# Kernel tuning notes

Measured on AMD Instinct MI355X. Metric: run time of the kernel, lower is better.

Reference implementation:

```python
import jax, jax.numpy as jnp
import numpy as np

L = 2        # NUM_DECODER_LAYERS
D = 512      # D_MODEL == ENCODER_EMBEDDING_DIM == DECODER_EMBEDDING_DIM == DECODER_HIDDEN_DIM
T = 32       # max_trg_len (greedy decode steps)
SOS = 1      # SPECIAL_TOKENS.index('[SOS]'), PAD assumed 0


def setup_inputs() -> dict:
    key = jax.random.key(0)
    ks = jax.random.split(key, 12)
    Vin, Vout, B, S = 32000, 32000, 32, 512
    s = 0.02
    src = jax.random.randint(ks[0], (B, S), 0, Vin)
    src_emb_table = jax.random.normal(ks[1], (Vin, D), dtype=jnp.float32) * s
    trg_emb_table = (jax.random.normal(ks[2], (Vout, D), dtype=jnp.float32) * s).at[0].set(0.0)  # padding_idx=0
    Wih = jax.random.normal(ks[3], (L, 4 * D, D), dtype=jnp.float32) * s
    Whh = jax.random.normal(ks[4], (L, 4 * D, D), dtype=jnp.float32) * s
    bih = jnp.zeros((L, 4 * D), jnp.float32)
    bhh = jnp.zeros((L, 4 * D), jnp.float32)
    Wfc = jax.random.normal(ks[5], (D, D), dtype=jnp.float32) * s      # Decoder.fc_out (hid_dim -> hid_dim)
    bfc = jnp.zeros((D,), jnp.float32)
    Wh2o = jax.random.normal(ks[6], (D, 2 * D), dtype=jnp.float32) * s  # hidden_to_out
    bh2o = jnp.zeros((D,), jnp.float32)
    bout = jnp.zeros((Vout,), jnp.float32)                              # out_layer bias (weight tied to trg_emb_table)
    return dict(src=src, src_emb_table=src_emb_table, trg_emb_table=trg_emb_table,
                Wih=Wih, Whh=Whh, bih=bih, bhh=bhh, Wfc=Wfc, bfc=bfc,
                Wh2o=Wh2o, bh2o=bh2o, bout=bout)


def reference(src, src_emb_table, trg_emb_table, Wih, Whh, bih, bhh, Wfc, bfc, Wh2o, bh2o, bout):
    B, S = src.shape
    dtype = src_emb_table.dtype
    scale = jnp.asarray(D ** 0.5, dtype)
    src_e = src_emb_table[src]  # [B,S,D] -- encoder LSTM hidden/cell are computed but discarded in the original

    def lstm_cell(x, h, c, l):
        g = x @ Wih[l].T + bih[l] + h @ Whh[l].T + bhh[l]
        i, f, gg, o = jnp.split(g, 4, axis=-1)  # torch gate order i,f,g,o
        c2 = jax.nn.sigmoid(f) * c + jax.nn.sigmoid(i) * jnp.tanh(gg)
        h2 = jax.nn.sigmoid(o) * jnp.tanh(c2)
        return h2, c2

    def outer_step(carry, t):
        # Original re-runs the decoder LSTM over the whole generated prefix every
        # step, starting from the carried hidden state; we mask positions > t.
        tokens, h, c = carry  # tokens [B,T+1] int32, h/c [L,B,D]
        emb = jnp.swapaxes(trg_emb_table[tokens[:, :T]], 0, 1)  # [T,B,D]

        def pos_step(hc, inp):
            h, c = hc
            x, pos = inp
            active = pos <= t
            hs, cs = [], []
            for l in range(L):
                h2, c2 = lstm_cell(x, h[l], c[l], l)
                h2 = jnp.where(active, h2, h[l])
                c2 = jnp.where(active, c2, c[l])
                hs.append(h2); cs.append(c2)
                x = h2
            h, c = jnp.stack(hs), jnp.stack(cs)
            return (h, c), h[-1]

        (h, c), h_top = jax.lax.scan(pos_step, (h, c), (emb, jnp.arange(T)))
        out_seq = h_top @ Wfc.T + bfc                 # [T,B,D] Decoder.fc_out
        out_t = jnp.take(out_seq, t, axis=0)          # last valid position (concat[:, -1])
        w = jax.nn.softmax(jnp.einsum('bd,bsd->bs', out_t, src_e) / scale, axis=-1)
        context = jnp.einsum('bs,bsd->bd', w, src_e)
        hid = jax.nn.relu(jnp.concatenate([out_t, context], axis=-1) @ Wh2o.T + bh2o)
        logits = hid @ trg_emb_table.T + bout         # out_layer tied to decoder embedding
        nxt = jnp.argmax(logits, axis=-1).astype(tokens.dtype)
        tokens = tokens.at[:, t + 1].set(nxt)
        return (tokens, h, c), out_seq

    tokens0 = jnp.zeros((B, T + 1), jnp.int32).at[:, 0].set(SOS)
    h0 = jnp.zeros((L, B, D), dtype)
    (tokens, _, _), out_seqs = jax.lax.scan(outer_step, (tokens0, h0, h0), jnp.arange(T))
    # attn returned by the original is from the LAST decode step, queries = all T positions
    attn = jax.nn.softmax(jnp.einsum('tbd,bsd->bts', out_seqs[-1], src_e) / scale, axis=-1)  # [B,T,S]
    return tokens[:, 1:], attn
```

## Files before the change

### kernel.cpp

```cpp
#include <hip/hip_runtime.h>
#include <math.h>

#define NWG 256
#define TPB 512
#define AGT __HIP_MEMORY_SCOPE_AGENT

static constexpr int Bb = 32, Dd = 512, Tt = 32, Vv = 32000;
static constexpr int BD = Bb * Dd;
static constexpr float SCALE_INV = 0.04419417382415922f;

static constexpr size_t OFF_H0 = 4096;
static constexpr size_t OFF_H1 = OFF_H0 + 2 * (size_t)BD;
static constexpr size_t OFF_P  = OFF_H1 + 2 * (size_t)BD;
static constexpr size_t OFF_HL = OFF_P + (size_t)Tt * Bb * 2048;
static constexpr size_t OFF_HD = OFF_HL + (size_t)Tt * BD;
static constexpr size_t OFF_OF = OFF_HD + BD;
static constexpr size_t OFF_CV = OFF_OF + (size_t)Tt * BD;
static constexpr size_t OFF_CI = OFF_CV + 32 * 256;
static constexpr size_t OFF_ET = OFF_CI + 32 * 256;

static constexpr int L_W   = 0;
static constexpr int L_H   = 13824;
static constexpr int L_SC  = 30208;
static constexpr int L_RB  = 30720;
static constexpr int L_IB  = 31744;
static constexpr int L_RED = 32256;
static constexpr int L_GV  = 32272;
static constexpr int L_GI  = 32400;
static constexpr int L_TOK = 32528;
static constexpr int LDS_FLOATS = 32560;
static constexpr size_t LDS_BYTES = (size_t)LDS_FLOATS * 4;

__device__ __forceinline__ float sigm(float x) { return 1.0f / (1.0f + expf(-x)); }

__device__ __forceinline__ float ldcv(const float* p) {
  unsigned u = __hip_atomic_load((const unsigned*)p, __ATOMIC_RELAXED, AGT);
  return __builtin_bit_cast(float, u);
}
__device__ __forceinline__ void stcv(float* p, float v) {
  __hip_atomic_store((unsigned*)p, __builtin_bit_cast(unsigned, v), __ATOMIC_RELAXED, AGT);
}
__device__ __forceinline__ float2 ldcv2(const float* p) {
  unsigned long long u = __hip_atomic_load((const unsigned long long*)p, __ATOMIC_RELAXED, AGT);
  return __builtin_bit_cast(float2, u);
}
__device__ __forceinline__ int ldcvi(const int* p) {
  return (int)__hip_atomic_load((const unsigned*)p, __ATOMIC_RELAXED, AGT);
}
__device__ __forceinline__ void stcvi(int* p, int v) {
  __hip_atomic_store((unsigned*)p, (unsigned)v, __ATOMIC_RELAXED, AGT);
}

__device__ __forceinline__ float wredsum(float v) {
#pragma unroll
  for (int off = 32; off > 0; off >>= 1) v += __shfl_xor(v, off, 64);
  return v;
}

__device__ __forceinline__ void gbar(unsigned* sb, unsigned& lg) {
  const unsigned tgt = lg + 1u;
  asm volatile("s_waitcnt vmcnt(0)" ::: "memory");
  __syncthreads();
  if (threadIdx.x == 0) {
    const int g = (int)blockIdx.x >> 5;
    unsigned a = __hip_atomic_fetch_add(&sb[g * 64], 1u, __ATOMIC_RELAXED, AGT);
    if (a == 31u) {
      __hip_atomic_store(&sb[g * 64], 0u, __ATOMIC_RELAXED, AGT);
      unsigned r = __hip_atomic_fetch_add(&sb[1024], 1u, __ATOMIC_RELAXED, AGT);
      if (r == 7u) {
        __hip_atomic_store(&sb[1024], 0u, __ATOMIC_RELAXED, AGT);
#pragma unroll
        for (int gg = 0; gg < 8; ++gg)
          __hip_atomic_store(&sb[2048 + gg * 64], tgt, __ATOMIC_RELAXED, AGT);
      }
    }
    while (__hip_atomic_load(&sb[2048 + g * 64], __ATOMIC_RELAXED, AGT) < tgt)
      __builtin_amdgcn_s_sleep(1);
  }
  lg = tgt;
  __syncthreads();
}

__device__ __forceinline__ float blockMax(float v, float* red, int tid) {
#pragma unroll
  for (int off = 32; off > 0; off >>= 1) v = fmaxf(v, __shfl_xor(v, off, 64));
  if ((tid & 63) == 0) red[tid >> 6] = v;
  __syncthreads();
  float m = red[0];
#pragma unroll
  for (int i = 1; i < 8; ++i) m = fmaxf(m, red[i]);
  __syncthreads();
  return m;
}

__device__ __forceinline__ float blockSum(float v, float* red, int tid) {
  v = wredsum(v);
  if ((tid & 63) == 0) red[tid >> 6] = v;
  __syncthreads();
  float s = 0.f;
#pragma unroll
  for (int i = 0; i < 8; ++i) s += red[i];
  __syncthreads();
  return s;
}

__device__ void stageW(int wg, int tid, const float* __restrict__ Wih,
                       const float* __restrict__ Whh, float* __restrict__ SMW) {
  for (int e = tid; e < 3 * 8 * 512; e += TPB) {
    const int k = e & 511, jl = (e >> 9) & 7, m = e >> 12;
    const int q = jl >> 1, dl = jl & 1;
    const int j = q * 512 + wg * 2 + dl;
    const float* srcp = (m == 0) ? (Whh + (size_t)j * 512)
                     : (m == 1) ? (Wih + (size_t)2048 * 512 + (size_t)j * 512)
                                : (Whh + (size_t)2048 * 512 + (size_t)j * 512);
    SMW[(m * 8 + jl) * 576 + (k >> 5) * 36 + (k & 31)] = srcp[k];
  }
  __syncthreads();
}

__device__ void buildETb(int wg, int tid, const float* __restrict__ Etrg,
                         float* __restrict__ ETb, float* __restrict__ SM) {
  if (wg < 250) {
    for (int tile = 0; tile < 8; ++tile) {
      const int tv = tile >> 2, tk = tile & 3;
      __syncthreads();
      for (int e = tid; e < 64 * 128; e += TPB) {
        const int vl = e >> 7, kl = e & 127;
        SM[vl * 129 + kl] = Etrg[(size_t)(wg * 128 + tv * 64 + vl) * 512 + tk * 128 + kl];
      }
      __syncthreads();
      for (int e = tid; e < 32 * 128; e += TPB) {
        const int vp = e >> 7, kl = e & 127;
        const int v = wg * 128 + tv * 64 + vp * 2;
        const int k = tk * 128 + kl;
        float2 val = make_float2(SM[(vp * 2) * 129 + kl], SM[(vp * 2 + 1) * 129 + kl]);
        *(float2*)(ETb + ((size_t)(v >> 1) * 512 + k) * 2) = val;
      }
    }
    __syncthreads();
  }
}

__device__ __forceinline__ void phaseAB(
    int wg, int tid, bool doA, bool doB,
    const float* __restrict__ H0r, float* __restrict__ H0w,
    const float* __restrict__ H1r, float* __restrict__ H1w,
    float* __restrict__ HlP, const float* __restrict__ Pp,
    const float* __restrict__ bs1,
    const float* __restrict__ SMW, float* __restrict__ LH, float& c0, float& c1)
{
  const int kc = tid & 15, b = tid >> 4;
  float4 s0[8], s1[8];
  __builtin_amdgcn_sched_barrier(0);
  {
    const float* p0 = H0r + tid * 4;
#pragma unroll
    for (int r = 0; r < 8; ++r) {
      const float* q = p0 + r * 2048;
      asm volatile("global_load_dwordx4 %0, %1, off sc1" : "=v"(s0[r]) : "v"(q));
    }
  }
  if (doB) {
    const float* p1 = H1r + tid * 4;
#pragma unroll
    for (int r = 0; r < 8; ++r) {
      const float* q = p1 + r * 2048;
      asm volatile("global_load_dwordx4 %0, %1, off sc1" : "=v"(s1[r]) : "v"(q));
    }
  }
  __builtin_amdgcn_sched_barrier(0);
  asm volatile("s_waitcnt vmcnt(0)" ::: "memory");
  __builtin_amdgcn_sched_barrier(0);
#pragma unroll
  for (int r = 0; r < 8; ++r) {
    int byte = (r * 512 + tid) * 16;
    byte ^= ((byte >> 7) & 7) << 4;
    *(float4*)((char*)LH + byte) = s0[r];
  }
  __syncthreads();
  float4 hq[8];
#pragma unroll
  for (int j = 0; j < 8; ++j) {
    int byte = tid * 128 + j * 16;
    byte ^= ((byte >> 7) & 7) << 4;
    hq[j] = *(const float4*)((const char*)LH + byte);
  }
  if (doB) {
    __syncthreads();
#pragma unroll
    for (int r = 0; r < 8; ++r) {
      int byte = (r * 512 + tid) * 16;
      byte ^= ((byte >> 7) & 7) << 4;
      *(float4*)((char*)LH + byte) = s1[r];
    }
  }
  float accA[8], accB[8];
#pragma unroll
  for (int r = 0; r < 8; ++r) { accA[r] = 0.f; accB[r] = 0.f; }
  if (doA) {
#pragma unroll
    for (int r = 0; r < 8; ++r) {
      const float4* wr = (const float4*)(SMW + r * 576 + kc * 36);
#pragma unroll
      for (int iq = 0; iq < 8; ++iq) {
        float4 w = wr[iq];
        accA[r] = fmaf(w.x, hq[iq].x, accA[r]);
        accA[r] = fmaf(w.y, hq[iq].y, accA[r]);
        accA[r] = fmaf(w.z, hq[iq].z, accA[r]);
        accA[r] = fmaf(w.w, hq[iq].w, accA[r]);
      }
    }
  }
  if (doB) {
#pragma unroll
    for (int r = 0; r < 8; ++r) {
      const float4* wr = (const float4*)(SMW + (8 + r) * 576 + kc * 36);
#pragma unroll
      for (int iq = 0; iq < 8; ++iq) {
        float4 w = wr[iq];
        accB[r] = fmaf(w.x, hq[iq].x, accB[r]);
        accB[r] = fmaf(w.y, hq[iq].y, accB[r]);
        accB[r] = fmaf(w.z, hq[iq].z, accB[r]);
        accB[r] = fmaf(w.w, hq[iq].w, accB[r]);
      }
    }
    __syncthreads();
#pragma unroll
    for (int j = 0; j < 8; ++j) {
      int byte = tid * 128 + j * 16;
      byte ^= ((byte >> 7) & 7) << 4;
      hq[j] = *(const float4*)((const char*)LH + byte);
    }
#pragma unroll
    for (int r = 0; r < 8; ++r) {
      const float4* wr = (const float4*)(SMW + (16 + r) * 576 + kc * 36);
#pragma unroll
      for (int iq = 0; iq < 8; ++iq) {
        float4 w = wr[iq];
        accB[r] = fmaf(w.x, hq[iq].x, accB[r]);
        accB[r] = fmaf(w.y, hq[iq].y, accB[r]);
        accB[r] = fmaf(w.z, hq[iq].z, accB[r]);
        accB[r] = fmaf(w.w, hq[iq].w, accB[r]);
      }
    }
  }
#pragma unroll
  for (int off = 1; off < 16; off <<= 1) {
    if (doA) {
#pragma unroll
      for (int r = 0; r < 8; ++r) accA[r] += __shfl_xor(accA[r], off, 64);
    }
    if (doB) {
#pragma unroll
      for (int r = 0; r < 8; ++r) accB[r] += __shfl_xor(accB[r], off, 64);
    }
  }
  if (kc < 2) {
    const int d = (wg << 1) | kc;
    if (doA) {
      const float* pb = Pp + b * 2048 + d;
      const float gi = accA[0 + kc] + pb[0];
      const float gf = accA[2 + kc] + pb[512];
      const float gg = accA[4 + kc] + pb[1024];
      const float go = accA[6 + kc] + pb[1536];
      c0 = sigm(gf) * c0 + sigm(gi) * tanhf(gg);
      stcv(H0w + b * 512 + d, sigm(go) * tanhf(c0));
    }
    if (doB) {
      const float gi = accB[0 + kc] + bs1[0];
      const float gf = accB[2 + kc] + bs1[1];
      const float gg = accB[4 + kc] + bs1[2];
      const float go = accB[6 + kc] + bs1[3];
      c1 = sigm(gf) * c1 + sigm(gi) * tanhf(gg);
      const float hn = sigm(go) * tanhf(c1);
      stcv(H1w + b * 512 + d, hn);
      if (HlP) stcv(HlP + b * 512 + d, hn);
    }
  }
}

__device__ void phaseCDEF(int b, int tid, const float* __restrict__ H1c,
                          const float* __restrict__ Wfc, const float* __restrict__ bfc,
                          const int* __restrict__ src, const float* __restrict__ Esrc,
                          const float* __restrict__ Wh2o, const float* __restrict__ bh2o,
                          float* __restrict__ hD, float* sc, float* rb, int* ib, float* red)
{
  rb[tid] = ldcv(H1c + b * 512 + tid);
  ib[tid] = src[b * 512 + tid];
  __syncthreads();
  const int w = tid >> 6, lane = tid & 63;
  for (int d = w; d < 512; d += 8) {
    const float* wr = Wfc + (size_t)d * 512;
    float p = 0.f;
#pragma unroll
    for (int i = 0; i < 8; ++i) p = fmaf(rb[lane * 8 + i], wr[lane * 8 + i], p);
    p = wredsum(p);
    if (lane == 0) rb[512 + d] = p + bfc[d];
  }
  __syncthreads();
  for (int s = w; s < 512; s += 8) {
    const float* er = Esrc + (size_t)ib[s] * 512;
    float p = 0.f;
#pragma unroll
    for (int i = 0; i < 8; ++i) p = fmaf(rb[512 + lane * 8 + i], er[lane * 8 + i], p);
    p = wredsum(p);
    if (lane == 0) sc[s] = p * SCALE_INV;
  }
  __syncthreads();
  const float mx = blockMax(sc[tid], red, tid);
  const float e = expf(sc[tid] - mx);
  sc[tid] = e;
  const float sum = blockSum(e, red, tid);
  const float inv = 1.0f / sum;
  float acc = 0.f;
#pragma unroll 4
  for (int s = 0; s < 512; ++s) acc = fmaf(sc[s], Esrc[(size_t)ib[s] * 512 + tid], acc);
  rb[tid] = acc * inv;
  __syncthreads();
  for (int d = w; d < 512; d += 8) {
    const float* wr = Wh2o + (size_t)d * 1024;
    float p = 0.f;
#pragma unroll
    for (int i = 0; i < 8; ++i) p = fmaf(rb[512 + lane * 8 + i], wr[lane * 8 + i], p);
#pragma unroll
    for (int i = 0; i < 8; ++i) p = fmaf(rb[lane * 8 + i], wr[512 + lane * 8 + i], p);
    p = wredsum(p);
    if (lane == 0) stcv(hD + (size_t)b * 512 + d, fmaxf(p + bh2o[d], 0.f));
  }
}

__device__ void phaseG_ET(int wg, int tid, const float* __restrict__ hD, const float* __restrict__ ETb,
                          const float* __restrict__ bout, float* __restrict__ candV,
                          int* __restrict__ candI, float* hidT, float* gv, int* gi)
{
  if (wg >= 250) return;
  const int v0 = wg * 128;
#pragma unroll 1
  for (int ph = 0; ph < 2; ++ph) {
    const int bbase = ph * 16;
    __syncthreads();
    for (int e = tid; e < 16 * 512; e += TPB) {
      const int bb = e >> 9, k = e & 511;
      hidT[k * 18 + bb] = ldcv(hD + (size_t)(bbase + bb) * 512 + k);
    }
    __syncthreads();
    const int vp = tid >> 3, bh = tid & 7;
    const int v = v0 + vp * 2;
    float a00 = 0.f, a01 = 0.f, a10 = 0.f, a11 = 0.f;
    const float* ep = ETb + (size_t)(v >> 1) * 1024;
    const float* hp = hidT + bh * 2;
#pragma unroll 8
    for (int k = 0; k < 512; ++k) {
      const float2 e2 = *(const float2*)(ep + k * 2);
      const float2 h2 = *(const float2*)(hp + k * 18);
      a00 = fmaf(e2.x, h2.x, a00);
      a01 = fmaf(e2.x, h2.y, a01);
      a10 = fmaf(e2.y, h2.x, a10);
      a11 = fmaf(e2.y, h2.y, a11);
    }
    const float bo0 = bout[v], bo1 = bout[v + 1];
    a00 += bo0; a01 += bo0; a10 += bo1; a11 += bo1;
    float vA, vB; int iA, iB;
    if (a10 > a00) { vA = a10; iA = v + 1; } else { vA = a00; iA = v; }
    if (a11 > a01) { vB = a11; iB = v + 1; } else { vB = a01; iB = v; }
#pragma unroll
    for (int off = 8; off < 64; off <<= 1) {
      float ov = __shfl_xor(vA, off, 64); int oi = __shfl_xor(iA, off, 64);
      if (ov > vA || (ov == vA && oi < iA)) { vA = ov; iA = oi; }
      ov = __shfl_xor(vB, off, 64); oi = __shfl_xor(iB, off, 64);
      if (ov > vB || (ov == vB && oi < iB)) { vB = ov; iB = oi; }
    }
    if ((tid & 63) < 8) {
      const int w = tid >> 6;
      gv[(bh * 2 + 0) * 8 + w] = vA; gi[(bh * 2 + 0) * 8 + w] = iA;
      gv[(bh * 2 + 1) * 8 + w] = vB; gi[(bh * 2 + 1) * 8 + w] = iB;
    }
    __syncthreads();
    if (tid < 16) {
      float bv = -INFINITY; int bi = 0;
      for (int w2 = 0; w2 < 8; ++w2) {
        const float vv = gv[tid * 8 + w2]; const int ii = gi[tid * 8 + w2];
        if (vv > bv || (vv == bv && ii < bi)) { bv = vv; bi = ii; }
      }
      stcv(candV + (size_t)(bbase + tid) * 256 + wg, bv);
      stcvi(candI + (bbase + tid) * 256 + wg, bi);
    }
  }
}

__device__ void phaseG_noET(int wg, int tid, const float* __restrict__ hD,
                            const float* __restrict__ Etrg, const float* __restrict__ bout,
                            float* __restrict__ candV, int* __restrict__ candI,
                            float* rb, float* gv, int* gi)
{
  const int b = wg >> 3, vb = wg & 7;
  rb[tid] = ldcv(hD + (size_t)b * 512 + tid);
  __syncthreads();
  const int w = tid >> 6, lane = tid & 63;
  float bv = -INFINITY; int bi = 0;
  for (int v = vb * 4000 + w; v < (vb + 1) * 4000; v += 8) {
    const float* er = Etrg + (size_t)v * 512;
    float p = 0.f;
#pragma unroll
    for (int i = 0; i < 8; ++i) p = fmaf(rb[lane * 8 + i], er[lane * 8 + i], p);
    p = wredsum(p);
    p += bout[v];
    if (p > bv || (p == bv && v < bi)) { bv = p; bi = v; }
  }
  if (lane == 0) { gv[w] = bv; gi[w] = bi; }
  __syncthreads();
  if (tid == 0) {
    float fv = -INFINITY; int fi = 0;
    for (int w2 = 0; w2 < 8; ++w2)
      if (gv[w2] > fv || (gv[w2] == fv && gi[w2] < fi)) { fv = gv[w2]; fi = gi[w2]; }
    stcv(candV + (size_t)b * 256 + vb, fv);
    stcvi(candI + b * 256 + vb, fi);
  }
  __syncthreads();
}

__device__ void phaseHP(int wg, int tid, int t, bool useET,
                        const float* __restrict__ candV, const int* __restrict__ candI,
                        const float* __restrict__ Etrg, const float* __restrict__ Wih,
                        const float* __restrict__ bih, const float* __restrict__ bhh,
                        float* __restrict__ P, float* __restrict__ out, int* tokL)
{
  const int nslot = useET ? 250 : 8;
  {
    const int b = tid >> 4, sl = tid & 15;
    float bv = -INFINITY; int bi = 0x7fffffff;
    for (int s = sl; s < nslot; s += 16) {
      const float vv = ldcv(candV + (size_t)b * 256 + s);
      const int ii = ldcvi(candI + b * 256 + s);
      if (vv > bv || (vv == bv && ii < bi)) { bv = vv; bi = ii; }
    }
#pragma unroll
    for (int off = 1; off < 16; off <<= 1) {
      const float ov = __shfl_xor(bv, off, 64); const int oi = __shfl_xor(bi, off, 64);
      if (ov > bv || (ov == bv && oi < bi)) { bv = ov; bi = oi; }
    }
    if (sl == 0) {
      tokL[b] = bi;
      if (wg == 0) out[b * 32 + t] = (float)bi;
    }
  }
  __syncthreads();
  if (t < 31) {
    const int w = tid >> 6, lane = tid & 63;
    const int q = w >> 1, dl = w & 1;
    const int j = q * 512 + wg * 2 + dl;
    const float* wr = Wih + (size_t)j * 512;
    const float bsum = bih[j] + bhh[j];
    for (int b = 0; b < 32; ++b) {
      const float* er = Etrg + (size_t)tokL[b] * 512;
      float p = 0.f;
#pragma unroll
      for (int i = 0; i < 8; ++i) p = fmaf(er[lane * 8 + i], wr[lane * 8 + i], p);
      p = wredsum(p);
      if (lane == 0) P[((size_t)(t + 1) * 32 + b) * 2048 + j] = p + bsum;
    }
  }
  __syncthreads();
}

__device__ void phaseX(int wg, int tid, const float* __restrict__ Hl, const float* __restrict__ Wfc,
                       const float* __restrict__ bfc, float* __restrict__ oF)
{
  const int p = wg >> 3, bq = wg & 7;
  const int w = tid >> 6, lane = tid & 63;
  for (int u = w; u < 2048; u += 8) {
    const int bb = u >> 9, d = u & 511;
    const int b = bq * 4 + bb;
    const float* hr = Hl + ((size_t)p * 32 + b) * 512;
    const float* wr = Wfc + (size_t)d * 512;
    float acc = 0.f;
#pragma unroll
    for (int ii = 0; ii < 4; ++ii) {
      const float2 hv = ldcv2(hr + lane * 8 + 2 * ii);
      acc = fmaf(hv.x, wr[lane * 8 + 2 * ii], acc);
      acc = fmaf(hv.y, wr[lane * 8 + 2 * ii + 1], acc);
    }
    acc = wredsum(acc);
    if (lane == 0) stcv(oF + ((size_t)p * 32 + b) * 512 + d, acc + bfc[d]);
  }
}

__device__ void phaseY(int wg, int tid, const float* __restrict__ oF, const int* __restrict__ src,
                       const float* __restrict__ Esrc, float* __restrict__ out,
                       float* sc, float* rb, int* ib, float* red)
{
  for (int r = 0; r < 4; ++r) {
    const int id = wg * 4 + r;
    const int b = id >> 5, p = id & 31;
    __syncthreads();
    rb[tid] = ldcv(oF + ((size_t)p * 32 + b) * 512 + tid);
    ib[tid] = src[b * 512 + tid];
    __syncthreads();
    const int w = tid >> 6, lane = tid & 63;
    for (int s = w; s < 512; s += 8) {
      const float* er = Esrc + (size_t)ib[s] * 512;
      float acc = 0.f;
#pragma unroll
      for (int i = 0; i < 8; ++i) acc = fmaf(rb[lane * 8 + i], er[lane * 8 + i], acc);
      acc = wredsum(acc);
      if (lane == 0) sc[s] = acc * SCALE_INV;
    }
    __syncthreads();
    const float mx = blockMax(sc[tid], red, tid);
    const float e = expf(sc[tid] - mx);
    const float sum = blockSum(e, red, tid);
    out[1024 + ((size_t)b * 32 + p) * 512 + tid] = e / sum;
  }
}

extern "C" __global__ void __launch_bounds__(TPB)
s2s_mega(const int* __restrict__ src, const float* __restrict__ Esrc, const float* __restrict__ Etrg,
         const float* __restrict__ Wih, const float* __restrict__ Whh,
         const float* __restrict__ bih, const float* __restrict__ bhh,
         const float* __restrict__ Wfc, const float* __restrict__ bfc,
         const float* __restrict__ Wh2o, const float* __restrict__ bh2o,
         const float* __restrict__ bout, float* __restrict__ out,
         float* __restrict__ ws, const float* __restrict__ ET, float* __restrict__ ETw)
{
  extern __shared__ float SM[];
  float* SMW = SM + L_W;
  float* LH  = SM + L_H;
  float* sc  = SM + L_SC;
  float* rb  = SM + L_RB;
  int*   ib  = (int*)(SM + L_IB);
  float* red = SM + L_RED;
  float* gv  = SM + L_GV;
  int*   gi  = (int*)(SM + L_GI);
  int*   tokL = (int*)(SM + L_TOK);

  unsigned* sb = (unsigned*)ws;
  float* H0 = ws + OFF_H0;
  float* H1 = ws + OFF_H1;
  float* P  = ws + OFF_P;
  float* Hl = ws + OFF_HL;
  float* hD = ws + OFF_HD;
  float* oF = ws + OFF_OF;
  float* cV = ws + OFF_CV;
  int*   cI = (int*)(ws + OFF_CI);

  const int wg = blockIdx.x, tid = threadIdx.x;
  const bool useET = (ET != nullptr);
  unsigned lg = 0u;
  float c0 = 0.f, c1 = 0.f;

  float bs1[4] = {0.f, 0.f, 0.f, 0.f};
  {
    const int kc = tid & 15;
    if (kc < 2) {
      const int d = (wg << 1) | kc;
#pragma unroll
      for (int q = 0; q < 4; ++q)
        bs1[q] = bih[2048 + q * 512 + d] + bhh[2048 + q * 512 + d];
    }
  }

  {
    const int gid = wg * TPB + tid;
    if (gid < BD) stcv(H0 + gid, 0.f);
    else if (gid < 2 * BD) stcv(H1 + gid - BD, 0.f);
  }
  {
    const int w = tid >> 6, lane = tid & 63;
    const int q = w >> 1, dl = w & 1;
    const int j = q * 512 + wg * 2 + dl;
    const float* er = Etrg + 512;
    const float* wr = Wih + (size_t)j * 512;
    float p = 0.f;
#pragma unroll
    for (int i = 0; i < 8; ++i) p = fmaf(er[lane * 8 + i], wr[lane * 8 + i], p);
    p = wredsum(p);
    p += bih[j] + bhh[j];
    if (lane < 32) P[(size_t)lane * 2048 + j] = p;
  }
  if (ETw) buildETb(wg, tid, Etrg, ETw, LH);
  stageW(wg, tid, Wih, Whh, SMW);
  gbar(sb, lg);

  int cur0 = 0, cur1 = 0;
  for (int t = 0; t < 32; ++t) {
    for (int k = 0; k <= t + 1; ++k) {
      const bool doA = (k <= t), doB = (k >= 1);
      float* HlP = (t == 31 && doB) ? (Hl + (size_t)(k - 1) * BD) : nullptr;
      const int kp = (k < 32) ? k : 31;
      phaseAB(wg, tid, doA, doB,
              H0 + (size_t)cur0 * BD, H0 + (size_t)(cur0 ^ 1) * BD,
              H1 + (size_t)cur1 * BD, H1 + (size_t)(cur1 ^ 1) * BD,
              HlP, P + (size_t)kp * Bb * 2048, bs1, SMW, LH, c0, c1);
      if (t >= 2 && k == 0) {
        if (useET) phaseG_ET(wg, tid, hD, ET, bout, cV, cI, LH, gv, gi);
        else       phaseG_noET(wg, tid, hD, Etrg, bout, cV, cI, rb, gv, gi);
      }
      if (t >= 2 && k == 1)
        phaseHP(wg, tid, t - 1, useET, cV, cI, Etrg, Wih, bih, bhh, P, out, tokL);
      gbar(sb, lg);
      if (doA) cur0 ^= 1;
      if (doB) cur1 ^= 1;
    }
    if (wg < 32) phaseCDEF(wg, tid, H1 + (size_t)cur1 * BD, Wfc, bfc, src, Esrc,
                           Wh2o, bh2o, hD, sc, rb, ib, red);
    gbar(sb, lg);
    if (t == 0) {
      if (useET) phaseG_ET(wg, tid, hD, ET, bout, cV, cI, LH, gv, gi);
      else       phaseG_noET(wg, tid, hD, Etrg, bout, cV, cI, rb, gv, gi);
      gbar(sb, lg);
      phaseHP(wg, tid, 0, useET, cV, cI, Etrg, Wih, bih, bhh, P, out, tokL);
      gbar(sb, lg);
    }
  }
  phaseX(wg, tid, Hl, Wfc, bfc, oF);
  if (useET) phaseG_ET(wg, tid, hD, ET, bout, cV, cI, LH, gv, gi);
  else       phaseG_noET(wg, tid, hD, Etrg, bout, cV, cI, rb, gv, gi);
  gbar(sb, lg);
  phaseHP(wg, tid, 31, useET, cV, cI, Etrg, Wih, bih, bhh, P, out, tokL);
  phaseY(wg, tid, oF, src, Esrc, out, sc, rb, ib, red);
}

extern "C" void kernel_launch(void* const* d_in, const int* in_sizes, int n_in,
                              void* d_out, int out_size, void* d_ws, size_t ws_size,
                              hipStream_t stream) {
  const int*   src  = (const int*)d_in[0];
  const float* Esrc = (const float*)d_in[1];
  const float* Etrg = (const float*)d_in[2];
  const float* Wih  = (const float*)d_in[3];
  const float* Whh  = (const float*)d_in[4];
  const float* bih  = (const float*)d_in[5];
  const float* bhh  = (const float*)d_in[6];
  const float* Wfc  = (const float*)d_in[7];
  const float* bfc  = (const float*)d_in[8];
  const float* Wh2o = (const float*)d_in[9];
  const float* bh2o = (const float*)d_in[10];
  const float* bout = (const float*)d_in[11];
  float* ws = (float*)d_ws;

  const size_t needET = (OFF_ET + (size_t)512 * 32000) * sizeof(float);
  const bool useET = (ws_size >= needET);
  float* etw = useET ? (ws + OFF_ET) : nullptr;

  hipMemsetAsync(d_ws, 0, 16384, stream);

  static bool attrDone = false;
  hipFuncSetAttribute(reinterpret_cast<const void*>(&s2s_mega),
                      hipFuncAttributeMaxDynamicSharedMemorySize, (int)LDS_BYTES);

  s2s_mega<<<dim3(NWG), dim3(TPB), LDS_BYTES, stream>>>(
      src, Esrc, Etrg, Wih, Whh, bih, bhh, Wfc, bfc, Wh2o, bh2o, bout,
      (float*)d_out, ws, etw, etw);
}
```

Before: 19.84 ms.

## Restructure LSTM gate matvec to two batches per thread with DPP reductions

Reworks the per-step LSTM gate computation so each thread handles two batch rows and one output column pair. Each weight float4 read from LDS is now reused across two batch rows, and the 16-lane partial sums are combined with DPP row operations instead of shuffles. The hidden-state layout in global memory is interleaved by batch pairs, and the consumers (fc_out, CDEF load) are updated to match. The second-layer hidden load now overlaps with the first dot products. In exchange there are more live registers (16 float4 of hidden state plus 12 accumulators) and a changed LDS swizzle, which could cost occupancy or add bank conflicts.

```diff
diff --git a/kernel.cpp b/kernel.cpp
--- a/kernel.cpp
+++ b/kernel.cpp
@@ -20,15 +20,15 @@
 static constexpr size_t OFF_ET = OFF_CI + 32 * 256;
 
 static constexpr int L_W   = 0;
-static constexpr int L_H   = 13824;
-static constexpr int L_SC  = 30208;
-static constexpr int L_RB  = 30720;
-static constexpr int L_IB  = 31744;
-static constexpr int L_RED = 32256;
-static constexpr int L_GV  = 32272;
-static constexpr int L_GI  = 32400;
-static constexpr int L_TOK = 32528;
-static constexpr int LDS_FLOATS = 32560;
+static constexpr int L_H   = 12288;
+static constexpr int L_SC  = 28672;
+static constexpr int L_RB  = 29184;
+static constexpr int L_IB  = 30208;
+static constexpr int L_RED = 30720;
+static constexpr int L_GV  = 30736;
+static constexpr int L_GI  = 30864;
+static constexpr int L_TOK = 30992;
+static constexpr int LDS_FLOATS = 31024;
 static constexpr size_t LDS_BYTES = (size_t)LDS_FLOATS * 4;
 
 __device__ __forceinline__ float sigm(float x) { return 1.0f / (1.0f + expf(-x)); }
@@ -56,6 +56,21 @@
   for (int off = 32; off > 0; off >>= 1) v += __shfl_xor(v, off, 64);
   return v;
 }
+
+__device__ __forceinline__ float rowReduce16(float x) {
+  int t;
+  t = __builtin_amdgcn_update_dpp(0, __builtin_bit_cast(int, x), 0x121, 0xF, 0xF, false);
+  x += __builtin_bit_cast(float, t);
+  t = __builtin_amdgcn_update_dpp(0, __builtin_bit_cast(int, x), 0x122, 0xF, 0xF, false);
+  x += __builtin_bit_cast(float, t);
+  t = __builtin_amdgcn_update_dpp(0, __builtin_bit_cast(int, x), 0x124, 0xF, 0xF, false);
+  x += __builtin_bit_cast(float, t);
+  t = __builtin_amdgcn_update_dpp(0, __builtin_bit_cast(int, x), 0x128, 0xF, 0xF, false);
+  x += __builtin_bit_cast(float, t);
+  return x;
+}
+
+__device__ __forceinline__ int swzH(int byte) { return byte ^ (((byte >> 8) & 7) << 4); }
 
 __device__ __forceinline__ void gbar(unsigned* sb, unsigned& lg) {
   const unsigned tgt = lg + 1u;
@@ -106,14 +121,14 @@
 
 __device__ void stageW(int wg, int tid, const float* __restrict__ Wih,
                        const float* __restrict__ Whh, float* __restrict__ SMW) {
-  for (int e = tid; e < 3 * 8 * 512; e += TPB) {
-    const int k = e & 511, jl = (e >> 9) & 7, m = e >> 12;
-    const int q = jl >> 1, dl = jl & 1;
+  for (int e = tid; e < 24 * 512; e += TPB) {
+    const int k = e & 511, rr = e >> 9;
+    const int m = rr >> 3, q = (rr >> 1) & 3, dl = rr & 1;
     const int j = q * 512 + wg * 2 + dl;
     const float* srcp = (m == 0) ? (Whh + (size_t)j * 512)
                      : (m == 1) ? (Wih + (size_t)2048 * 512 + (size_t)j * 512)
                                 : (Whh + (size_t)2048 * 512 + (size_t)j * 512);
-    SMW[(m * 8 + jl) * 576 + (k >> 5) * 36 + (k & 31)] = srcp[k];
+    SMW[rr * 512 + k] = srcp[k];
   }
   __syncthreads();
 }
@@ -141,140 +156,116 @@
   }
 }
 
+__device__ __forceinline__ void dotMQ(const float* __restrict__ SMW, int rr, int kc,
+                                      const float4* __restrict__ hq, float2& acc) {
+  const float4* wr = (const float4*)(SMW + rr * 512 + kc * 32);
+#pragma unroll
+  for (int i2 = 0; i2 < 8; ++i2) {
+    const float4 wv = wr[i2];
+    const float4 hA = hq[i2 * 2], hB = hq[i2 * 2 + 1];
+    acc.x = fmaf(wv.x, hA.x, acc.x); acc.y = fmaf(wv.x, hA.y, acc.y);
+    acc.x = fmaf(wv.y, hA.z, acc.x); acc.y = fmaf(wv.y, hA.w, acc.y);
+    acc.x = fmaf(wv.z, hB.x, acc.x); acc.y = fmaf(wv.z, hB.y, acc.y);
+    acc.x = fmaf(wv.w, hB.z, acc.x); acc.y = fmaf(wv.w, hB.w, acc.y);
+  }
+}
+
 __device__ __forceinline__ void phaseAB(
     int wg, int tid, bool doA, bool doB,
     const float* __restrict__ H0r, float* __restrict__ H0w,
     const float* __restrict__ H1r, float* __restrict__ H1w,
     float* __restrict__ HlP, const float* __restrict__ Pp,
-    const float* __restrict__ bs1,
-    const float* __restrict__ SMW, float* __restrict__ LH, float& c0, float& c1)
-{
-  const int kc = tid & 15, b = tid >> 4;
+    const float* __restrict__ bs1v,
+    const float* __restrict__ SMW, float* __restrict__ LH, float* c0, float* c1)
+{
+  const int b2 = tid >> 5, dl = (tid >> 4) & 1, kc = tid & 15;
+  char* LHc = (char*)LH;
   float4 s0[8], s1[8];
   __builtin_amdgcn_sched_barrier(0);
   {
     const float* p0 = H0r + tid * 4;
 #pragma unroll
-    for (int r = 0; r < 8; ++r) {
-      const float* q = p0 + r * 2048;
-      asm volatile("global_load_dwordx4 %0, %1, off sc1" : "=v"(s0[r]) : "v"(q));
-    }
+    for (int r = 0; r < 8; ++r)
+      asm volatile("global_load_dwordx4 %0, %1, off sc1" : "=v"(s0[r]) : "v"(p0 + r * 2048));
   }
   if (doB) {
     const float* p1 = H1r + tid * 4;
 #pragma unroll
-    for (int r = 0; r < 8; ++r) {
-      const float* q = p1 + r * 2048;
-      asm volatile("global_load_dwordx4 %0, %1, off sc1" : "=v"(s1[r]) : "v"(q));
-    }
+    for (int r = 0; r < 8; ++r)
+      asm volatile("global_load_dwordx4 %0, %1, off sc1" : "=v"(s1[r]) : "v"(p1 + r * 2048));
+    asm volatile("s_waitcnt vmcnt(8)" ::: "memory");
+  } else {
+    asm volatile("s_waitcnt vmcnt(0)" ::: "memory");
   }
   __builtin_amdgcn_sched_barrier(0);
-  asm volatile("s_waitcnt vmcnt(0)" ::: "memory");
-  __builtin_amdgcn_sched_barrier(0);
-#pragma unroll
-  for (int r = 0; r < 8; ++r) {
-    int byte = (r * 512 + tid) * 16;
-    byte ^= ((byte >> 7) & 7) << 4;
-    *(float4*)((char*)LH + byte) = s0[r];
-  }
-  __syncthreads();
-  float4 hq[8];
-#pragma unroll
-  for (int j = 0; j < 8; ++j) {
-    int byte = tid * 128 + j * 16;
-    byte ^= ((byte >> 7) & 7) << 4;
-    hq[j] = *(const float4*)((const char*)LH + byte);
+#pragma unroll
+  for (int r = 0; r < 8; ++r)
+    *(float4*)(LHc + swzH((r * 512 + tid) * 16)) = s0[r];
+  __syncthreads();
+  float4 hq[16];
+#pragma unroll
+  for (int i = 0; i < 16; ++i)
+    hq[i] = *(const float4*)(LHc + swzH(b2 * 4096 + kc * 256 + i * 16));
+
+  float2 acc2[12];
+#pragma unroll
+  for (int j = 0; j < 12; ++j) acc2[j] = make_float2(0.f, 0.f);
+
+  if (doA) {
+#pragma unroll
+    for (int q = 0; q < 4; ++q) dotMQ(SMW, q * 2 + dl, kc, hq, acc2[q]);
   }
   if (doB) {
-    __syncthreads();
-#pragma unroll
-    for (int r = 0; r < 8; ++r) {
-      int byte = (r * 512 + tid) * 16;
-      byte ^= ((byte >> 7) & 7) << 4;
-      *(float4*)((char*)LH + byte) = s1[r];
-    }
-  }
-  float accA[8], accB[8];
-#pragma unroll
-  for (int r = 0; r < 8; ++r) { accA[r] = 0.f; accB[r] = 0.f; }
-  if (doA) {
-#pragma unroll
-    for (int r = 0; r < 8; ++r) {
-      const float4* wr = (const float4*)(SMW + r * 576 + kc * 36);
-#pragma unroll
-      for (int iq = 0; iq < 8; ++iq) {
-        float4 w = wr[iq];
-        accA[r] = fmaf(w.x, hq[iq].x, accA[r]);
-        accA[r] = fmaf(w.y, hq[iq].y, accA[r]);
-        accA[r] = fmaf(w.z, hq[iq].z, accA[r]);
-        accA[r] = fmaf(w.w, hq[iq].w, accA[r]);
+#pragma unroll
+    for (int q = 0; q < 4; ++q) dotMQ(SMW, 8 + q * 2 + dl, kc, hq, acc2[4 + q]);
+    asm volatile("s_waitcnt vmcnt(0)" ::: "memory");
+    __builtin_amdgcn_sched_barrier(0);
+    __syncthreads();
+#pragma unroll
+    for (int r = 0; r < 8; ++r)
+      *(float4*)(LHc + swzH((r * 512 + tid) * 16)) = s1[r];
+    __syncthreads();
+#pragma unroll
+    for (int i = 0; i < 16; ++i)
+      hq[i] = *(const float4*)(LHc + swzH(b2 * 4096 + kc * 256 + i * 16));
+#pragma unroll
+    for (int q = 0; q < 4; ++q) dotMQ(SMW, 16 + q * 2 + dl, kc, hq, acc2[8 + q]);
+  }
+
+#pragma unroll
+  for (int j = 0; j < 12; ++j) {
+    if (j < 4 ? !doA : !doB) continue;
+    acc2[j].x = rowReduce16(acc2[j].x);
+    acc2[j].y = rowReduce16(acc2[j].y);
+  }
+
+  if (kc == 0) {
+    const int d = (wg << 1) | dl;
+    if (doA) {
+#pragma unroll
+      for (int p = 0; p < 2; ++p) {
+        const int b = b2 * 2 + p;
+        const float* pb = Pp + b * 2048 + d;
+        const float gi = (p ? acc2[0].y : acc2[0].x) + pb[0];
+        const float gf = (p ? acc2[1].y : acc2[1].x) + pb[512];
+        const float gg = (p ? acc2[2].y : acc2[2].x) + pb[1024];
+        const float go = (p ? acc2[3].y : acc2[3].x) + pb[1536];
+        c0[p] = sigm(gf) * c0[p] + sigm(gi) * tanhf(gg);
+        stcv(H0w + b2 * 1024 + d * 2 + p, sigm(go) * tanhf(c0[p]));
       }
     }
-  }
-  if (doB) {
-#pragma unroll
-    for (int r = 0; r < 8; ++r) {
-      const float4* wr = (const float4*)(SMW + (8 + r) * 576 + kc * 36);
-#pragma unroll
-      for (int iq = 0; iq < 8; ++iq) {
-        float4 w = wr[iq];
-        accB[r] = fmaf(w.x, hq[iq].x, accB[r]);
-        accB[r] = fmaf(w.y, hq[iq].y, accB[r]);
-        accB[r] = fmaf(w.z, hq[iq].z, accB[r]);
-        accB[r] = fmaf(w.w, hq[iq].w, accB[r]);
+    if (doB) {
+#pragma unroll
+      for (int p = 0; p < 2; ++p) {
+        const float gi = (p ? acc2[4].y : acc2[4].x) + (p ? acc2[8].y  : acc2[8].x)  + bs1v[0];
+        const float gf = (p ? acc2[5].y : acc2[5].x) + (p ? acc2[9].y  : acc2[9].x)  + bs1v[1];
+        const float gg = (p ? acc2[6].y : acc2[6].x) + (p ? acc2[10].y : acc2[10].x) + bs1v[2];
+        const float go = (p ? acc2[7].y : acc2[7].x) + (p ? acc2[11].y : acc2[11].x) + bs1v[3];
+        c1[p] = sigm(gf) * c1[p] + sigm(gi) * tanhf(gg);
+        const float hn = sigm(go) * tanhf(c1[p]);
+        stcv(H1w + b2 * 1024 + d * 2 + p, hn);
+        if (HlP) stcv(HlP + b2 * 1024 + d * 2 + p, hn);
       }
-    }
-    __syncthreads();
-#pragma unroll
-    for (int j = 0; j < 8; ++j) {
-      int byte = tid * 128 + j * 16;
-      byte ^= ((byte >> 7) & 7) << 4;
-      hq[j] = *(const float4*)((const char*)LH + byte);
-    }
-#pragma unroll
-    for (int r = 0; r < 8; ++r) {
-      const float4* wr = (const float4*)(SMW + (16 + r) * 576 + kc * 36);
-#pragma unroll
-      for (int iq = 0; iq < 8; ++iq) {
-        float4 w = wr[iq];
-        accB[r] = fmaf(w.x, hq[iq].x, accB[r]);
-        accB[r] = fmaf(w.y, hq[iq].y, accB[r]);
-        accB[r] = fmaf(w.z, hq[iq].z, accB[r]);
-        accB[r] = fmaf(w.w, hq[iq].w, accB[r]);
-      }
-    }
-  }
-#pragma unroll
-  for (int off = 1; off < 16; off <<= 1) {
-    if (doA) {
-#pragma unroll
-      for (int r = 0; r < 8; ++r) accA[r] += __shfl_xor(accA[r], off, 64);
-    }
-    if (doB) {
-#pragma unroll
-      for (int r = 0; r < 8; ++r) accB[r] += __shfl_xor(accB[r], off, 64);
-    }
-  }
-  if (kc < 2) {
-    const int d = (wg << 1) | kc;
-    if (doA) {
-      const float* pb = Pp + b * 2048 + d;
-      const float gi = accA[0 + kc] + pb[0];
-      const float gf = accA[2 + kc] + pb[512];
-      const float gg = accA[4 + kc] + pb[1024];
-      const float go = accA[6 + kc] + pb[1536];
-      c0 = sigm(gf) * c0 + sigm(gi) * tanhf(gg);
-      stcv(H0w + b * 512 + d, sigm(go) * tanhf(c0));
-    }
-    if (doB) {
-      const float gi = accB[0 + kc] + bs1[0];
-      const float gf = accB[2 + kc] + bs1[1];
-      const float gg = accB[4 + kc] + bs1[2];
-      const float go = accB[6 + kc] + bs1[3];
-      c1 = sigm(gf) * c1 + sigm(gi) * tanhf(gg);
-      const float hn = sigm(go) * tanhf(c1);
-      stcv(H1w + b * 512 + d, hn);
-      if (HlP) stcv(HlP + b * 512 + d, hn);
     }
   }
 }
@@ -285,7 +276,7 @@
                           const float* __restrict__ Wh2o, const float* __restrict__ bh2o,
                           float* __restrict__ hD, float* sc, float* rb, int* ib, float* red)
 {
-  rb[tid] = ldcv(H1c + b * 512 + tid);
+  rb[tid] = ldcv(H1c + (b >> 1) * 1024 + tid * 2 + (b & 1));
   ib[tid] = src[b * 512 + tid];
   __syncthreads();
   const int w = tid >> 6, lane = tid & 63;
@@ -468,20 +459,23 @@
 {
   const int p = wg >> 3, bq = wg & 7;
   const int w = tid >> 6, lane = tid & 63;
-  for (int u = w; u < 2048; u += 8) {
-    const int bb = u >> 9, d = u & 511;
-    const int b = bq * 4 + bb;
-    const float* hr = Hl + ((size_t)p * 32 + b) * 512;
+  for (int u = w; u < 1024; u += 8) {
+    const int b2 = bq * 2 + (u >> 9), d = u & 511;
+    const float* hr = Hl + (size_t)p * BD + b2 * 1024;
     const float* wr = Wfc + (size_t)d * 512;
-    float acc = 0.f;
-#pragma unroll
-    for (int ii = 0; ii < 4; ++ii) {
-      const float2 hv = ldcv2(hr + lane * 8 + 2 * ii);
-      acc = fmaf(hv.x, wr[lane * 8 + 2 * ii], acc);
-      acc = fmaf(hv.y, wr[lane * 8 + 2 * ii + 1], acc);
-    }
-    acc = wredsum(acc);
-    if (lane == 0) stcv(oF + ((size_t)p * 32 + b) * 512 + d, acc + bfc[d]);
+    float ax = 0.f, ay = 0.f;
+#pragma unroll
+    for (int i = 0; i < 8; ++i) {
+      const float2 hv = ldcv2(hr + (lane * 8 + i) * 2);
+      const float wv = wr[lane * 8 + i];
+      ax = fmaf(hv.x, wv, ax);
+      ay = fmaf(hv.y, wv, ay);
+    }
+    ax = wredsum(ax); ay = wredsum(ay);
+    if (lane == 0) {
+      stcv(oF + ((size_t)p * 32 + b2 * 2    ) * 512 + d, ax + bfc[d]);
+      stcv(oF + ((size_t)p * 32 + b2 * 2 + 1) * 512 + d, ay + bfc[d]);
+    }
   }
 }
 
@@ -546,17 +540,15 @@
   const int wg = blockIdx.x, tid = threadIdx.x;
   const bool useET = (ET != nullptr);
   unsigned lg = 0u;
-  float c0 = 0.f, c1 = 0.f;
-
-  float bs1[4] = {0.f, 0.f, 0.f, 0.f};
+  float c0[2] = {0.f, 0.f}, c1[2] = {0.f, 0.f};
+
+  float bs1v[4];
   {
-    const int kc = tid & 15;
-    if (kc < 2) {
-      const int d = (wg << 1) | kc;
-#pragma unroll
-      for (int q = 0; q < 4; ++q)
-        bs1[q] = bih[2048 + q * 512 + d] + bhh[2048 + q * 512 + d];
-    }
+    const int dl = (tid >> 4) & 1;
+    const int d = (wg << 1) | dl;
+#pragma unroll
+    for (int q = 0; q < 4; ++q)
+      bs1v[q] = bih[2048 + q * 512 + d] + bhh[2048 + q * 512 + d];
   }
 
   {
@@ -590,7 +582,7 @@
       phaseAB(wg, tid, doA, doB,
               H0 + (size_t)cur0 * BD, H0 + (size_t)(cur0 ^ 1) * BD,
               H1 + (size_t)cur1 * BD, H1 + (size_t)(cur1 ^ 1) * BD,
-              HlP, P + (size_t)kp * Bb * 2048, bs1, SMW, LH, c0, c1);
+              HlP, P + (size_t)kp * Bb * 2048, bs1v, SMW, LH, c0, c1);
       if (t >= 2 && k == 0) {
         if (useET) phaseG_ET(wg, tid, hD, ET, bout, cV, cI, LH, gv, gi);
         else       phaseG_noET(wg, tid, hD, Etrg, bout, cV, cI, rb, gv, gi);
@@ -641,11 +633,10 @@
   const bool useET = (ws_size >= needET);
   float* etw = useET ? (ws + OFF_ET) : nullptr;
 
-  hipMemsetAsync(d_ws, 0, 16384, stream);
-
-  static bool attrDone = false;
-  hipFuncSetAttribute(reinterpret_cast<const void*>(&s2s_mega),
-                      hipFuncAttributeMaxDynamicSharedMemorySize, (int)LDS_BYTES);
+  (void)hipMemsetAsync(d_ws, 0, 16384, stream);
+
+  (void)hipFuncSetAttribute(reinterpret_cast<const void*>(&s2s_mega),
+                            hipFuncAttributeMaxDynamicSharedMemorySize, (int)LDS_BYTES);
 
   s2s_mega<<<dim3(NWG), dim3(TPB), LDS_BYTES, stream>>>(
       src, Esrc, Etrg, Wih, Whh, bih, bhh, Wfc, bfc, Wh2o, bh2o, bout,
```

Result: slower. 22.67 ms (+14.3%).
